# Kernel tuning notes

Hardware: AMD Instinct MI355X
Metric: run time of the kernel (lower is better)

The kernel has to match this reference:

```python
import jax, jax.numpy as jnp
import numpy as np
from math import sqrt

EMBED_DIM = 1024
NUM_HEADS = 16
HEAD_DIM = EMBED_DIM // NUM_HEADS  # 64
SCALE = sqrt(HEAD_DIM)


def _rotate_half(x):
    # matches torch: stack((-x[...,1::2], x[...,0::2]), -1).flatten(-2)
    x1 = x[..., 0::2]
    x2 = x[..., 1::2]
    return jnp.stack((-x2, x1), axis=-1).reshape(x.shape)


def _apply_rope(x, seq_len):
    # x: [B, H, S, D]
    inv_freq = 1.0 / (10000.0 ** (jnp.arange(0, HEAD_DIM, 2, dtype=jnp.float32) / HEAD_DIM))
    pos = jnp.arange(seq_len, dtype=jnp.float32)
    freqs = jnp.outer(pos, inv_freq)            # [S, D/2]
    emb = jnp.concatenate([freqs, freqs], -1)   # [S, D]
    cos = jnp.cos(emb)[None, None].astype(x.dtype)
    sin = jnp.sin(emb)[None, None].astype(x.dtype)
    return x * cos + _rotate_half(x) * sin


def setup_inputs() -> dict:
    key = jax.random.key(0)
    ks = jax.random.split(key, 9)
    B, S, E = 2, 2048, EMBED_DIM
    s = 1.0 / np.sqrt(E)
    return {
        "x": jax.random.normal(ks[0], (B, S, E), jnp.float32),
        "Wq": jax.random.uniform(ks[1], (E, E), jnp.float32, -s, s),
        "bq": jnp.zeros((E,), jnp.float32),
        "Wk": jax.random.uniform(ks[2], (E, E), jnp.float32, -s, s),
        "bk": jnp.zeros((E,), jnp.float32),
        "Wv": jax.random.uniform(ks[3], (E, E), jnp.float32, -s, s),
        "bv": jnp.zeros((E,), jnp.float32),
        "Wo": jax.random.uniform(ks[4], (E, E), jnp.float32, -s, s),
        "bo": jnp.zeros((E,), jnp.float32),
    }


def reference(x, Wq, bq, Wk, bk, Wv, bv, Wo, bo):
    B, S, E = x.shape
    H, D = NUM_HEADS, HEAD_DIM
    # projections (torch Linear: x @ W.T + b), split heads -> [B, H, S, D]
    q = (x @ Wq.T + bq).reshape(B, S, H, D).transpose(0, 2, 1, 3)
    k = (x @ Wk.T + bk).reshape(B, S, H, D).transpose(0, 2, 1, 3)
    v = (x @ Wv.T + bv).reshape(B, S, H, D).transpose(0, 2, 1, 3)
    q = _apply_rope(q, S)
    k = _apply_rope(k, S)
    attn = jnp.einsum("bhqd,bhkd->bhqk", q, k) / SCALE
    attn = jax.nn.softmax(attn, axis=-1)
    out = jnp.einsum("bhqk,bhkd->bhqd", attn, v)
    out = out.transpose(0, 2, 1, 3).reshape(B, S, E)
    return out @ Wo.T + bo
```

## Files before the change

kernel.cpp:

```cpp
#include <hip/hip_runtime.h>
#include <hip/hip_bf16.h>
#include <math.h>

typedef __bf16 bf16;
typedef __bf16 bf16x4 __attribute__((ext_vector_type(4)));
typedef __bf16 bf16x8 __attribute__((ext_vector_type(8)));
typedef float f32x4 __attribute__((ext_vector_type(4)));

#define SEQ  2048
#define EMB  1024
#define NH   16
#define HD   64
#define MTOT 4096

__device__ __forceinline__ void gl_lds16(const void* g, void* l) {
  __builtin_amdgcn_global_load_lds(
      (const __attribute__((address_space(1))) void*)g,
      (__attribute__((address_space(3))) void*)l, 16, 0, 0);
}

__device__ __forceinline__ f32x4 mfma16(bf16x8 a, bf16x8 b, f32x4 c) {
  return __builtin_amdgcn_mfma_f32_16x16x32_bf16(a, b, c, 0, 0, 0);
}

#define ROPE_C 0.41524101186092026f
#define QSCL  0.1803368801111244f

__global__ __launch_bounds__(256) void cvt_all_kernel(
    const float* __restrict__ x,
    const float* __restrict__ w0, const float* __restrict__ w1,
    const float* __restrict__ w2, const float* __restrict__ w3,
    bf16* __restrict__ dst) {
  const int y = blockIdx.y;
  const size_t WN = (size_t)EMB * EMB;
  const float* src = (y < 4) ? (x + (size_t)y * WN)
                   : (y == 4) ? w0 : (y == 5) ? w1 : (y == 6) ? w2 : w3;
  size_t i = ((size_t)blockIdx.x * 256 + threadIdx.x) * 8;
  float4 a = *(const float4*)(src + i);
  float4 b = *(const float4*)(src + i + 4);
  bf16x8 o;
  o[0] = (bf16)a.x; o[1] = (bf16)a.y; o[2] = (bf16)a.z; o[3] = (bf16)a.w;
  o[4] = (bf16)b.x; o[5] = (bf16)b.y; o[6] = (bf16)b.z; o[7] = (bf16)b.w;
  *(bf16x8*)(dst + (size_t)y * WN + i) = o;
}

__global__ __launch_bounds__(256) void gemm_kernel(
    const bf16* __restrict__ X,
    const bf16* __restrict__ W0, const bf16* __restrict__ W1, const bf16* __restrict__ W2,
    const float* __restrict__ B0, const float* __restrict__ B1, const float* __restrict__ B2,
    bf16* __restrict__ Oq, bf16* __restrict__ Ok, bf16* __restrict__ Ovt)
{
  const int K = EMB;
  const int tid  = threadIdx.x;
  const int lane = tid & 63;
  const int w    = tid >> 6;
  const int wm   = w >> 1, wn = w & 1;
  const int lin = blockIdx.x + blockIdx.y * 16;
  const int sw  = (lin & 7) * 64 + (lin >> 3);
  const int tile_n = (sw & 15) * 64;
  const int tile_m = (sw >> 4) * 128;
  const int z = blockIdx.z;
  const bf16*  Wsel = (z == 0) ? W0 : (z == 1 ? W1 : W2);
  const float* Bsel = (z == 0) ? B0 : (z == 1 ? B1 : B2);

  __shared__ __align__(16) unsigned char smem[24576];
  bf16* As = (bf16*)smem;
  bf16* Bs = (bf16*)(smem + 16384);

  f32x4 acc[4][2];
#pragma unroll
  for (int i = 0; i < 4; i++)
#pragma unroll
    for (int j = 0; j < 2; j++) acc[i][j] = f32x4{0.f, 0.f, 0.f, 0.f};

  const int quad  = lane >> 4;
  const int l15   = lane & 15;
  const int srow8 = lane >> 3;
  const int p8    = lane & 7;
  const int csrc  = p8 ^ srow8;

  for (int k0 = 0; k0 < K; k0 += 64) {
#pragma unroll
    for (int i = 0; i < 4; i++) {
      const int ii = w * 4 + i;
      const int r  = ii * 8 + srow8;
      gl_lds16(X + (size_t)(tile_m + r) * K + k0 + csrc * 8, As + ii * 512);
    }
#pragma unroll
    for (int i = 0; i < 2; i++) {
      const int ii = w * 2 + i;
      const int r  = ii * 8 + srow8;
      gl_lds16(Wsel + (size_t)(tile_n + r) * K + k0 + csrc * 8, Bs + ii * 512);
    }
    __syncthreads();

#pragma unroll
    for (int kk = 0; kk < 2; kk++) {
      bf16x8 af[4], bfr[2];
#pragma unroll
      for (int mt = 0; mt < 4; mt++) {
        int ml = wm * 64 + mt * 16 + l15;
        af[mt] = *(const bf16x8*)(As + ml * 64 + (((kk * 4 + quad) ^ (ml & 7)) & 7) * 8);
      }
#pragma unroll
      for (int nt = 0; nt < 2; nt++) {
        int nl = wn * 32 + nt * 16 + l15;
        bfr[nt] = *(const bf16x8*)(Bs + nl * 64 + (((kk * 4 + quad) ^ (nl & 7)) & 7) * 8);
      }
#pragma unroll
      for (int mt = 0; mt < 4; mt++)
#pragma unroll
        for (int nt = 0; nt < 2; nt++)
          acc[mt][nt] = mfma16(af[mt], bfr[nt], acc[mt][nt]);
    }
    __syncthreads();
  }

  bf16* CS = (bf16*)smem;
  const int b  = tile_m >> 11;
  const int s0 = tile_m & (SEQ - 1);
  const int hg = tile_n >> 6;

  if (z < 2) {
#pragma unroll
    for (int nt = 0; nt < 2; nt++) {
      const int nl = wn * 32 + nt * 16 + l15;
      const int n = tile_n + nl;
      const float bias = Bsel[n];
      const int j = n & 31;
      const float invf = exp2f(-(float)j * ROPE_C);
#pragma unroll
      for (int mt = 0; mt < 4; mt++) {
#pragma unroll
        for (int r = 0; r < 4; r++) {
          const int ml = wm * 64 + mt * 16 + quad * 4 + r;
          float a = acc[mt][nt][r] + bias;
          float p = __shfl_xor(a, 1, 64);
          float th = (float)(s0 + ml) * invf;
          float sn, cs;
          __sincosf(th, &sn, &cs);
          float res = (n & 1) ? fmaf(p, sn, a * cs) : fmaf(-p, sn, a * cs);
          if (z == 0) res *= QSCL;
          CS[ml * 72 + nl] = (bf16)res;
        }
      }
    }
    __syncthreads();
    bf16* Odst = (z == 0) ? Oq : Ok;
#pragma unroll
    for (int g = 0; g < 4; g++) {
      int unit = g * 256 + tid;
      int chunk = unit & 7;
      int row = unit >> 3;
      bf16x8 v = *(const bf16x8*)(CS + row * 72 + chunk * 8);
      size_t o = ((size_t)(b * NH + hg) * SEQ + s0 + row) * HD + chunk * 8;
      *(bf16x8*)(Odst + o) = v;
    }
  } else {
#pragma unroll
    for (int nt = 0; nt < 2; nt++) {
      const int nl = wn * 32 + nt * 16 + l15;
      const float bias = Bsel[tile_n + nl];
#pragma unroll
      for (int mt = 0; mt < 4; mt++) {
        const int mb = wm * 64 + mt * 16 + quad * 4;
#pragma unroll
        for (int r = 0; r < 4; r++) {
          const int ml = mb + r;
          const int mp = (ml & ~31) | ((ml & 12) << 1) | ((ml & 16) >> 2) | (ml & 3);
          CS[nl * 132 + mp] = (bf16)(acc[mt][nt][r] + bias);
        }
      }
    }
    __syncthreads();
#pragma unroll
    for (int g = 0; g < 4; g++) {
      int unit = g * 256 + tid;
      int chunk = unit & 15;
      int row = unit >> 4;
      bf16x8 v = *(const bf16x8*)(CS + row * 132 + chunk * 8);
      size_t o = ((size_t)(b * NH + hg) * HD + row) * SEQ + s0 + chunk * 8;
      *(bf16x8*)(Ovt + o) = v;
    }
  }
}

__global__ __launch_bounds__(256) void gemm_o_kernel(
    const bf16* __restrict__ X,
    const bf16* __restrict__ W,
    const float* __restrict__ Bb,
    float* __restrict__ Out)
{
  const int tid = threadIdx.x, lane = tid & 63, w = tid >> 6;
  const int lin = blockIdx.x + blockIdx.y * 8;
  const int sw  = (lin & 7) * 64 + (lin >> 3);
  const int tile_n = (sw & 7) * 128;
  const int tile_m = (sw >> 3) * 64;
  __shared__ __align__(16) unsigned char smem[49152];
  bf16* As = (bf16*)smem;
  bf16* Bs = (bf16*)(smem + 16384);

  f32x4 acc[4][2];
#pragma unroll
  for (int i = 0; i < 4; i++)
#pragma unroll
    for (int j = 0; j < 2; j++) acc[i][j] = f32x4{0.f, 0.f, 0.f, 0.f};

  const int quad = lane >> 4, l15 = lane & 15;
  const int srow4 = lane >> 4;
  const int p16   = lane & 15;

  for (int k0 = 0; k0 < EMB; k0 += 128) {
#pragma unroll
    for (int i = 0; i < 4; i++) {
      int r = (w * 4 + i) * 4 + srow4;
      int c = p16 ^ (r & 15);
      gl_lds16(X + (size_t)(tile_m + r) * EMB + k0 + c * 8, As + (w * 4 + i) * 512);
    }
#pragma unroll
    for (int i = 0; i < 8; i++) {
      int r = (w * 8 + i) * 4 + srow4;
      int c = p16 ^ (r & 15);
      gl_lds16(W + (size_t)(tile_n + r) * EMB + k0 + c * 8, Bs + (w * 8 + i) * 512);
    }
    __syncthreads();

#pragma unroll
    for (int kk = 0; kk < 4; kk++) {
      bf16x8 af[4], bfr[2];
#pragma unroll
      for (int mt = 0; mt < 4; mt++) {
        int ml = mt * 16 + l15;
        af[mt] = *(const bf16x8*)(As + ml * 128 + (((kk * 4 + quad) ^ (ml & 15)) & 15) * 8);
      }
#pragma unroll
      for (int nt = 0; nt < 2; nt++) {
        int nl = w * 32 + nt * 16 + l15;
        bfr[nt] = *(const bf16x8*)(Bs + nl * 128 + (((kk * 4 + quad) ^ (nl & 15)) & 15) * 8);
      }
#pragma unroll
      for (int mt = 0; mt < 4; mt++)
#pragma unroll
        for (int nt = 0; nt < 2; nt++)
          acc[mt][nt] = mfma16(af[mt], bfr[nt], acc[mt][nt]);
    }
    __syncthreads();
  }

  float* CSf = (float*)smem;
#pragma unroll
  for (int nt = 0; nt < 2; nt++) {
    const int nl = w * 32 + nt * 16 + l15;
    const float bias = Bb[tile_n + nl];
#pragma unroll
    for (int mt = 0; mt < 4; mt++)
#pragma unroll
      for (int r = 0; r < 4; r++)
        CSf[(mt * 16 + quad * 4 + r) * 132 + nl] = acc[mt][nt][r] + bias;
  }
  __syncthreads();
#pragma unroll
  for (int g = 0; g < 8; g++) {
    int unit = g * 256 + tid;
    int chunk = unit & 31;
    int row = unit >> 5;
    float4 v = *(const float4*)(CSf + row * 132 + chunk * 4);
    *(float4*)(Out + (size_t)(tile_m + row) * EMB + tile_n + chunk * 4) = v;
  }
}

__global__ __launch_bounds__(256) void flash_kernel(
    const bf16* __restrict__ Q,
    const bf16* __restrict__ Kk,
    const bf16* __restrict__ Vt,
    bf16* __restrict__ O)
{
  const int lin = blockIdx.x + blockIdx.y * 16;
  const int sw  = (lin & 7) * 64 + (lin >> 3);
  const int bh  = sw >> 4;
  const int qt  = sw & 15;
  const int tid = threadIdx.x, lane = tid & 63, w = tid >> 6;
  const int quad = lane >> 4, l15 = lane & 15;

  __shared__ __align__(16) unsigned char smem[65536];

  const bf16* qbase = Q  + (size_t)bh * SEQ * HD;
  const bf16* kbase = Kk + (size_t)bh * SEQ * HD;
  const bf16* vbase = Vt + (size_t)bh * HD * SEQ;

  auto stage = [&](int kt, int buf) {
    bf16* Ks = (bf16*)(smem + buf * 32768);
    bf16* Vs = Ks + 8192;
#pragma unroll
    for (int i = 0; i < 4; i++) {
      int r = w * 32 + i * 8 + (lane >> 3);
      int c = (lane & 7) ^ (r & 7);
      gl_lds16(kbase + (size_t)(kt * 128 + r) * HD + c * 8, Ks + (w * 32 + i * 8) * 64);
      int dv = w * 16 + i * 4 + (lane >> 4);
      int cv = (lane & 15) ^ (dv & 15);
      gl_lds16(vbase + (size_t)dv * SEQ + kt * 128 + cv * 8, Vs + (w * 16 + i * 4) * 128);
    }
  };

  stage(0, 0);

  bf16x8 qf[2][2];
#pragma unroll
  for (int m = 0; m < 2; m++)
#pragma unroll
    for (int t = 0; t < 2; t++)
      qf[m][t] = *(const bf16x8*)(qbase + (size_t)(qt * 128 + w * 32 + m * 16 + l15) * HD
                                  + t * 32 + quad * 8);

  bf16x8 ones;
#pragma unroll
  for (int i = 0; i < 8; i++) ones[i] = (bf16)1.0f;

  f32x4 lacc[2];
  f32x4 oacc[2][4];
#pragma unroll
  for (int m = 0; m < 2; m++) {
    lacc[m] = f32x4{0.f, 0.f, 0.f, 0.f};
#pragma unroll
    for (int i = 0; i < 4; i++) oacc[m][i] = f32x4{0.f, 0.f, 0.f, 0.f};
  }

  __syncthreads();

  for (int kt = 0; kt < SEQ / 128; kt++) {
    const int buf = kt & 1;
    if (kt + 1 < SEQ / 128) stage(kt + 1, buf ^ 1);
    const bf16* Ks = (const bf16*)(smem + buf * 32768);
    const bf16* Vs = Ks + 8192;

    __builtin_amdgcn_s_setprio(1);
#pragma unroll
    for (int t2 = 0; t2 < 4; t2++) {
      bf16x8 pa[2];
#pragma unroll
      for (int hh = 0; hh < 2; hh++) {
        const int krow = (t2 * 2 + hh) * 16 + l15;
        const int swz = krow & 7;
        bf16x8 kf0 = *(const bf16x8*)(Ks + krow * 64 + ((quad ^ swz) & 7) * 8);
        bf16x8 kf1 = *(const bf16x8*)(Ks + krow * 64 + (((4 + quad) ^ swz) & 7) * 8);
#pragma unroll
        for (int mq = 0; mq < 2; mq++) {
          f32x4 s = f32x4{0.f, 0.f, 0.f, 0.f};
          s = mfma16(kf0, qf[mq][0], s);
          s = mfma16(kf1, qf[mq][1], s);
#pragma unroll
          for (int r = 0; r < 4; r++)
            pa[mq][hh * 4 + r] = (bf16)__builtin_amdgcn_exp2f(s[r]);
        }
      }
#pragma unroll
      for (int dt = 0; dt < 4; dt++) {
        const int d = dt * 16 + l15;
        bf16x8 vv = *(const bf16x8*)(Vs + d * 128 + ((t2 * 4 + quad) ^ l15) * 8);
#pragma unroll
        for (int mq = 0; mq < 2; mq++)
          oacc[mq][dt] = mfma16(vv, pa[mq], oacc[mq][dt]);
      }
#pragma unroll
      for (int mq = 0; mq < 2; mq++)
        lacc[mq] = mfma16(ones, pa[mq], lacc[mq]);
    }
    __builtin_amdgcn_s_setprio(0);
    __syncthreads();
  }

  float rls[2];
#pragma unroll
  for (int mq = 0; mq < 2; mq++)
    rls[mq] = __builtin_amdgcn_rcpf(lacc[mq][0]);

  const int b = bh >> 4, h = bh & 15;
#pragma unroll
  for (int mq = 0; mq < 2; mq++) {
    const int srow = qt * 128 + w * 32 + mq * 16 + l15;
    bf16* orow = O + ((size_t)(b * SEQ + srow)) * EMB + h * HD;
#pragma unroll
    for (int dt = 0; dt < 4; dt++) {
      bf16x4 ov;
#pragma unroll
      for (int r = 0; r < 4; r++) ov[r] = (bf16)(oacc[mq][dt][r] * rls[mq]);
      *(bf16x4*)(orow + dt * 16 + quad * 4) = ov;
    }
  }
}

extern "C" void kernel_launch(void* const* d_in, const int* in_sizes, int n_in,
                              void* d_out, int out_size, void* d_ws, size_t ws_size,
                              hipStream_t stream) {
  const float* x  = (const float*)d_in[0];
  const float* Wq = (const float*)d_in[1];
  const float* bq = (const float*)d_in[2];
  const float* Wk = (const float*)d_in[3];
  const float* bk = (const float*)d_in[4];
  const float* Wv = (const float*)d_in[5];
  const float* bv = (const float*)d_in[6];
  const float* Wo = (const float*)d_in[7];
  const float* bo = (const float*)d_in[8];

  const size_t XN = (size_t)MTOT * EMB;
  const size_t WN = (size_t)EMB * EMB;

  bf16* xb = (bf16*)d_ws;
  bf16* wq = xb + XN;
  bf16* wk = wq + WN;
  bf16* wv = wk + WN;
  bf16* wo = wv + WN;
  bf16* q  = wo + WN;
  bf16* k  = q + XN;
  bf16* vt = k + XN;
  bf16* at = vt + XN;
  float* out = (float*)d_out;

  dim3 blk(256);
  cvt_all_kernel<<<dim3(512, 8), blk, 0, stream>>>(x, Wq, Wk, Wv, Wo, xb);

  gemm_kernel<<<dim3(16, 32, 3), blk, 0, stream>>>(
      xb, wq, wk, wv, bq, bk, bv, q, k, vt);
  flash_kernel<<<dim3(16, 32), blk, 0, stream>>>(q, k, vt, at);
  gemm_o_kernel<<<dim3(8, 64), blk, 0, stream>>>(at, wo, bo, out);
}
```

Baseline: 179.2 us.

## Retile output projection GEMM to 128x64 tiles with 2x2 warp layout

The output-projection GEMM moves from 64x128 block tiles with a K step of 128 to 128x64 tiles with a K step of 64. The four warps are arranged 2x2 over M and N, and the XOR swizzle is adapted to 8-chunk rows. LDS use drops from 48KB to 24KB, which should allow more resident blocks per CU. The LDS-staged coalesced float4 epilogue is replaced by direct scalar stores from registers, which saves LDS traffic and a barrier but writes less coalesced global memory.

```diff
diff --git a/kernel.cpp b/kernel.cpp
--- a/kernel.cpp
+++ b/kernel.cpp
@@ -191,12 +191,16 @@
     const float* __restrict__ Bb,
     float* __restrict__ Out)
 {
-  const int tid = threadIdx.x, lane = tid & 63, w = tid >> 6;
-  const int lin = blockIdx.x + blockIdx.y * 8;
+  const int tid  = threadIdx.x;
+  const int lane = tid & 63;
+  const int w    = tid >> 6;
+  const int wm   = w >> 1, wn = w & 1;
+  const int lin = blockIdx.x + blockIdx.y * 16;
   const int sw  = (lin & 7) * 64 + (lin >> 3);
-  const int tile_n = (sw & 7) * 128;
-  const int tile_m = (sw >> 3) * 64;
-  __shared__ __align__(16) unsigned char smem[49152];
+  const int tile_n = (sw & 15) * 64;
+  const int tile_m = (sw >> 4) * 128;
+
+  __shared__ __align__(16) unsigned char smem[24576];
   bf16* As = (bf16*)smem;
   bf16* Bs = (bf16*)(smem + 16384);
 
@@ -206,37 +210,39 @@
 #pragma unroll
     for (int j = 0; j < 2; j++) acc[i][j] = f32x4{0.f, 0.f, 0.f, 0.f};
 
-  const int quad = lane >> 4, l15 = lane & 15;
-  const int srow4 = lane >> 4;
-  const int p16   = lane & 15;
-
-  for (int k0 = 0; k0 < EMB; k0 += 128) {
+  const int quad  = lane >> 4;
+  const int l15   = lane & 15;
+  const int srow8 = lane >> 3;
+  const int p8    = lane & 7;
+  const int csrc  = p8 ^ srow8;
+
+  for (int k0 = 0; k0 < EMB; k0 += 64) {
 #pragma unroll
     for (int i = 0; i < 4; i++) {
-      int r = (w * 4 + i) * 4 + srow4;
-      int c = p16 ^ (r & 15);
-      gl_lds16(X + (size_t)(tile_m + r) * EMB + k0 + c * 8, As + (w * 4 + i) * 512);
-    }
-#pragma unroll
-    for (int i = 0; i < 8; i++) {
-      int r = (w * 8 + i) * 4 + srow4;
-      int c = p16 ^ (r & 15);
-      gl_lds16(W + (size_t)(tile_n + r) * EMB + k0 + c * 8, Bs + (w * 8 + i) * 512);
-    }
-    __syncthreads();
-
-#pragma unroll
-    for (int kk = 0; kk < 4; kk++) {
+      const int ii = w * 4 + i;
+      const int r  = ii * 8 + srow8;
+      gl_lds16(X + (size_t)(tile_m + r) * EMB + k0 + csrc * 8, As + ii * 512);
+    }
+#pragma unroll
+    for (int i = 0; i < 2; i++) {
+      const int ii = w * 2 + i;
+      const int r  = ii * 8 + srow8;
+      gl_lds16(W + (size_t)(tile_n + r) * EMB + k0 + csrc * 8, Bs + ii * 512);
+    }
+    __syncthreads();
+
+#pragma unroll
+    for (int kk = 0; kk < 2; kk++) {
       bf16x8 af[4], bfr[2];
 #pragma unroll
       for (int mt = 0; mt < 4; mt++) {
-        int ml = mt * 16 + l15;
-        af[mt] = *(const bf16x8*)(As + ml * 128 + (((kk * 4 + quad) ^ (ml & 15)) & 15) * 8);
+        int ml = wm * 64 + mt * 16 + l15;
+        af[mt] = *(const bf16x8*)(As + ml * 64 + (((kk * 4 + quad) ^ (ml & 7)) & 7) * 8);
       }
 #pragma unroll
       for (int nt = 0; nt < 2; nt++) {
-        int nl = w * 32 + nt * 16 + l15;
-        bfr[nt] = *(const bf16x8*)(Bs + nl * 128 + (((kk * 4 + quad) ^ (nl & 15)) & 15) * 8);
+        int nl = wn * 32 + nt * 16 + l15;
+        bfr[nt] = *(const bf16x8*)(Bs + nl * 64 + (((kk * 4 + quad) ^ (nl & 7)) & 7) * 8);
       }
 #pragma unroll
       for (int mt = 0; mt < 4; mt++)
@@ -247,25 +253,18 @@
     __syncthreads();
   }
 
-  float* CSf = (float*)smem;
 #pragma unroll
   for (int nt = 0; nt < 2; nt++) {
-    const int nl = w * 32 + nt * 16 + l15;
-    const float bias = Bb[tile_n + nl];
-#pragma unroll
-    for (int mt = 0; mt < 4; mt++)
-#pragma unroll
-      for (int r = 0; r < 4; r++)
-        CSf[(mt * 16 + quad * 4 + r) * 132 + nl] = acc[mt][nt][r] + bias;
-  }
-  __syncthreads();
-#pragma unroll
-  for (int g = 0; g < 8; g++) {
-    int unit = g * 256 + tid;
-    int chunk = unit & 31;
-    int row = unit >> 5;
-    float4 v = *(const float4*)(CSf + row * 132 + chunk * 4);
-    *(float4*)(Out + (size_t)(tile_m + row) * EMB + tile_n + chunk * 4) = v;
+    const int n = tile_n + wn * 32 + nt * 16 + l15;
+    const float bias = Bb[n];
+#pragma unroll
+    for (int mt = 0; mt < 4; mt++) {
+#pragma unroll
+      for (int r = 0; r < 4; r++) {
+        const int m = tile_m + wm * 64 + mt * 16 + quad * 4 + r;
+        Out[(size_t)m * EMB + n] = acc[mt][nt][r] + bias;
+      }
+    }
   }
 }
 
@@ -422,5 +421,5 @@
   gemm_kernel<<<dim3(16, 32, 3), blk, 0, stream>>>(
       xb, wq, wk, wv, bq, bk, bv, q, k, vt);
   flash_kernel<<<dim3(16, 32), blk, 0, stream>>>(q, k, vt, at);
-  gemm_o_kernel<<<dim3(8, 64), blk, 0, stream>>>(at, wo, bo, out);
-}
+  gemm_o_kernel<<<dim3(16, 32), blk, 0, stream>>>(at, wo, bo, out);
+}
```

Result: no change. 178.4 us (-0.5%).
